# Kernel tuning notes

Hardware: AMD Instinct MI355X
Metric: run time of the kernel (lower is better)

The kernel has to match this reference:

```python
import jax, jax.numpy as jnp
import numpy as np

EPS = 1e-5

def _ln(x, g, b):
    mu = x.mean(-1, keepdims=True)
    var = ((x - mu) ** 2).mean(-1, keepdims=True)
    return (x - mu) * jax.lax.rsqrt(var + EPS) * g + b

def setup_inputs() -> dict:
    B, K, D, H, T = 64, 64, 128, 128, 4
    key = jax.random.key(0)
    ks = jax.random.split(key, 20)
    s = 0.02
    inp = {
        "slots": jax.random.normal(ks[0], (B, K, D), jnp.float32),
        "edge_probs": jax.random.uniform(ks[1], (B, K, K), jnp.float32),
        "edge_types": jax.random.uniform(ks[2], (B, K, K, T), jnp.float32),
        # f_self: LayerNorm(D) -> Linear(D,H) -> ReLU -> Linear(H,D)
        "ls_g": jnp.ones((D,), jnp.float32),
        "ls_b": jnp.zeros((D,), jnp.float32),
        "ws1": jax.random.normal(ks[3], (D, H), jnp.float32) * s,
        "bs1": jnp.zeros((H,), jnp.float32),
        "ws2": jax.random.normal(ks[4], (H, D), jnp.float32) * s,
        "bs2": jnp.zeros((D,), jnp.float32),
        # f_inter[tau]: Linear(2D,H) -> ReLU -> Linear(H,H) -> ReLU -> Linear(H,D), stacked over T
        "wi1": jax.random.normal(ks[5], (T, 2 * D, H), jnp.float32) * s,
        "bi1": jnp.zeros((T, H), jnp.float32),
        "wi2": jax.random.normal(ks[6], (T, H, H), jnp.float32) * s,
        "bi2": jnp.zeros((T, H), jnp.float32),
        "wi3": jax.random.normal(ks[7], (T, H, D), jnp.float32) * s,
        "bi3": jnp.zeros((T, D), jnp.float32),
        # update_mlp: LayerNorm(2D) -> Linear(2D,H) -> ReLU -> Linear(H,D)
        "lu_g": jnp.ones((2 * D,), jnp.float32),
        "lu_b": jnp.zeros((2 * D,), jnp.float32),
        "wu1": jax.random.normal(ks[8], (2 * D, H), jnp.float32) * s,
        "bu1": jnp.zeros((H,), jnp.float32),
        "wu2": jax.random.normal(ks[9], (H, D), jnp.float32) * s,
        "bu2": jnp.zeros((D,), jnp.float32),
    }
    return inp

NUM_MP = 2

def reference(slots, edge_probs, edge_types, ls_g, ls_b, ws1, bs1, ws2, bs2,
              wi1, bi1, wi2, bi2, wi3, bi3, lu_g, lu_b, wu1, bu1, wu2, bu2):
    B, K, D = slots.shape
    T = edge_types.shape[-1]
    h = slots
    for _ in range(NUM_MP):
        # f_self
        delta_self = jax.nn.relu(_ln(h, ls_g, ls_b) @ ws1 + bs1) @ ws2 + bs2
        # all-pairs features: cat[b,i,j] = [h[b,i] (sender), h[b,j] (receiver)]
        sender = jnp.broadcast_to(h[:, :, None, :], (B, K, K, D))
        receiver = jnp.broadcast_to(h[:, None, :, :], (B, K, K, D))
        pair = jnp.concatenate([sender, receiver], axis=-1)  # [B,K,K,2D]
        delta_inter = jnp.zeros_like(h)
        for tau in range(T):
            x = jax.nn.relu(pair @ wi1[tau] + bi1[tau])
            x = jax.nn.relu(x @ wi2[tau] + bi2[tau])
            eff = x @ wi3[tau] + bi3[tau]  # [B,K,K,D]
            w = edge_probs[..., None] * edge_types[..., tau, None]  # [B,K,K,1]
            delta_inter = delta_inter + (eff * w).sum(axis=1)  # sum over sender i
        combined = jnp.concatenate([h + delta_self, delta_inter], axis=-1)
        update = jax.nn.relu(_ln(combined, lu_g, lu_b) @ wu1 + bu1) @ wu2 + bu2
        h = h + update  # residual=True
    return h
```

## Files before the change

### kernel.cpp

```cpp
#include <hip/hip_runtime.h>
#include <hip/hip_fp16.h>

#define BATCH 64
#define KSLOT 64
#define DDIM  128
#define HDIM  128
#define TTYPE 4
#define NSLOT (BATCH*KSLOT)
#define EPSLN 1e-5f
#define YROW  544

typedef _Float16 v8h __attribute__((ext_vector_type(8)));
typedef _Float16 v4h __attribute__((ext_vector_type(4)));
typedef _Float16 v2h __attribute__((ext_vector_type(2)));
typedef float    v4f __attribute__((ext_vector_type(4)));

__device__ __forceinline__ float waveAllSum(float v) {
    #pragma unroll
    for (int m = 1; m < 64; m <<= 1) v += __shfl_xor(v, m, 64);
    return v;
}

__global__ __launch_bounds__(256) void k_wconv(
        const float* __restrict__ ws1, const float* __restrict__ wi1,
        const float* __restrict__ ws2, const float* __restrict__ wu1,
        const float* __restrict__ wu2, const float* __restrict__ wi3,
        const float* __restrict__ wi2, const float* __restrict__ bi1,
        const float* __restrict__ bi3,
        const float* __restrict__ ep, const float* __restrict__ et,
        __half* __restrict__ ws1T, __half* __restrict__ wi1catT,
        __half* __restrict__ ws2T, __half* __restrict__ wu1T,
        __half* __restrict__ wu2T, __half* __restrict__ w3catT,
        __half* __restrict__ w2T16, float* __restrict__ biascat,
        __half* __restrict__ wPre) {
    __shared__ __align__(16) float tile[128*132];
    int bx = blockIdx.x, tid = threadIdx.x;
    if (bx >= 22) {
        int bx2 = bx - 22, tau = bx2 & 3, b = bx2 >> 2;
        const float* epb = ep + (size_t)b*4096;
        const float* etb = et + (size_t)b*4096*TTYPE + tau;
        __half* dst = wPre + ((size_t)tau*BATCH + b)*4096;
        for (int idx = tid; idx < 4096; idx += 256)
            dst[idx] = __float2half(epb[idx] * etb[(size_t)idx*TTYPE]);
        return;
    }
    if (bx == 21) {
        for (int idx = tid; idx < 128*32; idx += 256) {
            int o = idx >> 5, c = idx & 31;
            w3catT[(size_t)o*YROW + 512 + c] = (c < 4) ? __float2half(bi3[c*DDIM + o]) : __float2half(0.f);
        }
        for (int idx = tid; idx < 1024; idx += 256) {
            int th = idx >> 7, o = idx & 127;
            biascat[idx] = (th & 1) ? bi1[(th>>1)*HDIM + o] : 0.f;
        }
        return;
    }
    const float* src; __half* dst; int dstride = 128, dcol = 0;
    if (bx == 0)      { src = ws1; dst = ws1T; }
    else if (bx <= 8) { int th = bx-1, tau = th>>1, half = th&1;
                        src = wi1 + ((size_t)tau*256 + half*128)*128;
                        dst = wi1catT + (size_t)th*128*128; }
    else if (bx == 9) { src = ws2; dst = ws2T; }
    else if (bx ==10) { src = wu2; dst = wu2T; }
    else if (bx <=12) { int hh = bx-11; src = wu1 + (size_t)hh*128*128;
                        dst = wu1T; dstride = 256; dcol = hh*128; }
    else if (bx <=16) { int tau = bx-13; src = wi3 + (size_t)tau*16384;
                        dst = w3catT; dstride = YROW; dcol = tau*128; }
    else              { int tau = bx-17; src = wi2 + (size_t)tau*16384;
                        dst = w2T16 + (size_t)tau*16384; }
    for (int idx = tid; idx < 4096; idx += 256) {
        int r = idx >> 5, c4 = idx & 31;
        *(float4*)&tile[r*132 + c4*4] = *(const float4*)&src[(size_t)r*128 + c4*4];
    }
    __syncthreads();
    for (int idx = tid; idx < 8192; idx += 256) {
        int n = idx >> 6, kp = idx & 63;
        __half2 p = __floats2half2_rn(tile[(2*kp)*132 + n], tile[(2*kp+1)*132 + n]);
        *(__half2*)&dst[(size_t)n*dstride + dcol + 2*kp] = p;
    }
}

#define LROW 136
__global__ __launch_bounds__(512, 4) void k_pair(
        const float* __restrict__ h,
        const __half* __restrict__ wi1catT,
        const float* __restrict__ biascat,
        const __half* __restrict__ w2T16,
        const float* __restrict__ bi2,
        const __half* __restrict__ wPre,
        __half* __restrict__ Ycat) {
    __shared__ __align__(16) _Float16 U[HDIM*LROW];
    __shared__ __align__(16) _Float16 Cs[32*LROW];
    __shared__ __align__(16) _Float16 As[KSLOT*LROW];
    __shared__ __align__(16) _Float16 wS[KSLOT*32];
    int bx = blockIdx.x;
    int jhalf = bx & 1, tau = (bx >> 1) & 3, b = bx >> 3;
    int tid = threadIdx.x, lane = tid & 63, w = tid >> 6;
    int quad = lane >> 4, n = lane & 15;
    int jt = w >> 2, oh = (w >> 1) & 1, otg = w & 1;

    v8h wreg[4];
    #pragma unroll
    for (int k2 = 0; k2 < 4; k2++) {
        int idx = tid + k2*512;
        int o = idx >> 4, seg = (idx & 15)*8;
        wreg[k2] = *(const v8h*)&w2T16[((size_t)tau*128 + o)*128 + seg];
    }
    {
        int row = tid >> 3, c0 = (tid & 7)*16;
        const float* hp = &h[(size_t)(b*KSLOT + row)*128 + c0];
        #pragma unroll
        for (int q = 0; q < 4; q++) {
            float4 f = *(const float4*)&hp[q*4];
            *(__half2*)&U[row*LROW + c0 + q*4]     = __floats2half2_rn(f.x, f.y);
            *(__half2*)&U[row*LROW + c0 + q*4 + 2] = __floats2half2_rn(f.z, f.w);
        }
    }
    if (tid < 256) {
        int i = tid >> 2, seg = (tid & 3)*8;
        *(v8h*)&wS[i*32 + seg] =
            *(const v8h*)&wPre[((size_t)tau*BATCH + b)*4096 + i*64 + jhalf*32 + seg];
    }
    __syncthreads();

    if (w < 6) {
        int isA = (w < 4);
        int rt  = isA ? w : (w - 4);
        int hrow0 = isA ? rt*16 : (jhalf*32 + rt*16);
        const __half* wb = wi1catT + (size_t)(tau*2 + (isA ? 0 : 1))*128*128;
        const float* bcp = biascat + (tau*2 + (isA ? 0 : 1))*128;
        _Float16* dst = isA ? (As + rt*16*LROW) : (Cs + rt*16*LROW);
        v8h afr[4];
        #pragma unroll
        for (int ks = 0; ks < 4; ks++)
            afr[ks] = *(const v8h*)&U[(hrow0 + n)*LROW + ks*32 + quad*8];
        #pragma unroll
        for (int ot = 0; ot < 8; ot++) {
            float b0 = bcp[ot*16 + n];
            v4f acc = (v4f){b0, b0, b0, b0};
            #pragma unroll
            for (int ks = 0; ks < 4; ks++)
                acc = __builtin_amdgcn_mfma_f32_16x16x32_f16(
                    afr[ks], *(const v8h*)&wb[(size_t)(ot*16 + n)*128 + ks*32 + quad*8], acc, 0, 0, 0);
            #pragma unroll
            for (int r = 0; r < 4; r++)
                dst[(quad*4 + r)*LROW + ot*16 + n] = (_Float16)acc[r];
        }
    }
    __syncthreads();
    #pragma unroll
    for (int k2 = 0; k2 < 4; k2++) {
        int idx = tid + k2*512;
        int o = idx >> 4, seg = (idx & 15)*8;
        *(v8h*)&U[o*LROW + seg] = wreg[k2];
    }
    __syncthreads();

    v8h bfrag[2][4];
    #pragma unroll
    for (int ot = 0; ot < 2; ot++)
        #pragma unroll
        for (int ks = 0; ks < 4; ks++)
            bfrag[ot][ks] = *(const v8h*)&U[(oh*64 + otg*32 + ot*16 + n)*LROW + ks*32 + quad*8];
    v8h cfrag[4];
    #pragma unroll
    for (int ks = 0; ks < 4; ks++)
        cfrag[ks] = *(const v8h*)&Cs[(jt*16 + n)*LROW + ks*32 + quad*8];
    v4f biasvec[2];
    #pragma unroll
    for (int ot = 0; ot < 2; ot++) {
        float b0 = bi2[tau*HDIM + oh*64 + otg*32 + ot*16 + n];
        biasvec[ot] = (v4f){b0, b0, b0, b0};
    }

    v4h yacch[2];
    #pragma unroll
    for (int ot = 0; ot < 2; ot++) yacch[ot] = (v4h){0,0,0,0};
    v4h wsacch = (v4h){0,0,0,0};
    const v8h zero8 = {0,0,0,0,0,0,0,0};
    const v4h zero4h = {0,0,0,0};

    v8h aN[4]; v4h wvN;
    #pragma unroll
    for (int ks = 0; ks < 4; ks++) aN[ks] = *(const v8h*)&As[ks*32 + quad*8];
    wvN = *(const v4h*)&wS[jt*16 + quad*4];

    for (int i = 0; i < KSLOT; ++i) {
        v8h a[4]; v4h wv = wvN;
        #pragma unroll
        for (int ks = 0; ks < 4; ks++) a[ks] = aN[ks];
        if (i < KSLOT-1) {
            #pragma unroll
            for (int ks = 0; ks < 4; ks++)
                aN[ks] = *(const v8h*)&As[(i+1)*LROW + ks*32 + quad*8];
            wvN = *(const v4h*)&wS[(i+1)*32 + jt*16 + quad*4];
        }
        v8h x1[4];
        #pragma unroll
        for (int ks = 0; ks < 4; ks++)
            x1[ks] = __builtin_elementwise_max(a[ks] + cfrag[ks], zero8);
        #pragma unroll
        for (int ot = 0; ot < 2; ot++) {
            v4f acc = __builtin_amdgcn_mfma_f32_16x16x32_f16(x1[0], bfrag[ot][0], biasvec[ot], 0, 0, 0);
            #pragma unroll
            for (int ks = 1; ks < 4; ks++)
                acc = __builtin_amdgcn_mfma_f32_16x16x32_f16(x1[ks], bfrag[ot][ks], acc, 0, 0, 0);
            v2h lo = __builtin_bit_cast(v2h, __builtin_amdgcn_cvt_pkrtz(acc[0], acc[1]));
            v2h hi = __builtin_bit_cast(v2h, __builtin_amdgcn_cvt_pkrtz(acc[2], acc[3]));
            v4h rel = {lo[0], lo[1], hi[0], hi[1]};
            rel = __builtin_elementwise_max(rel, zero4h);
            yacch[ot] = yacch[ot] + wv * rel;
        }
        wsacch = wsacch + wv;
    }

    #pragma unroll
    for (int r = 0; r < 4; r++) {
        int j = jhalf*32 + jt*16 + quad*4 + r;
        __half* yb = Ycat + (size_t)(b*KSLOT + j)*YROW + tau*128 + oh*64 + otg*32;
        #pragma unroll
        for (int ot = 0; ot < 2; ot++)
            yb[ot*16 + n] = __float2half((float)yacch[ot][r]);
    }
    if (oh == 0 && otg == 0 && n == 0) {
        #pragma unroll
        for (int r = 0; r < 4; r++) {
            int j = jhalf*32 + jt*16 + quad*4 + r;
            Ycat[(size_t)(b*KSLOT + j)*YROW + 512 + tau] = __float2half((float)wsacch[r]);
        }
    }
    if (tau == 0 && oh == 1 && otg == 1 && n == 0) {
        const v4h z4 = {0,0,0,0};
        #pragma unroll
        for (int r = 0; r < 4; r++) {
            int j = jhalf*32 + jt*16 + quad*4 + r;
            _Float16* pz = (_Float16*)(Ycat + (size_t)(b*KSLOT + j)*YROW + 516);
            #pragma unroll
            for (int c = 0; c < 28; c += 4) *(v4h*)&pz[c] = z4;
        }
    }
}

__global__ __launch_bounds__(512, 1) void k_mega(
        const __half* __restrict__ Ycat, const __half* __restrict__ w3catT,
        const float* __restrict__ ls_g, const float* __restrict__ ls_b,
        const __half* __restrict__ ws1T, const float* __restrict__ bs1,
        const __half* __restrict__ ws2T, const float* __restrict__ bs2,
        const float* __restrict__ g, const float* __restrict__ bb,
        const __half* __restrict__ wu1T, const float* __restrict__ bu1,
        const __half* __restrict__ wu2T, const float* __restrict__ bu2,
        const float* __restrict__ h, float* __restrict__ hout) {
    __shared__ __align__(16) _Float16 Ys[16*552];
    __shared__ __align__(16) float    Crow[16*260];
    __shared__ __align__(16) float    Hrow[16*132];
    __shared__ __align__(16) _Float16 Xs[16*136];
    __shared__ __align__(16) _Float16 Ts[16*136];
    __shared__ __align__(16) _Float16 Xa[16*264];
    __shared__ __align__(16) _Float16 Ut[16*136];
    int tid = threadIdx.x, lane = tid & 63, w = tid >> 6;
    int n = lane & 15, quad = lane >> 4;
    int row0 = blockIdx.x*16;
    v8h f3[17];
    #pragma unroll
    for (int ks = 0; ks < 17; ks++)
        f3[ks] = *(const v8h*)&w3catT[(size_t)(w*16 + n)*YROW + ks*32 + quad*8];
    v8h f1[8];
    #pragma unroll
    for (int ks = 0; ks < 8; ks++)
        f1[ks] = *(const v8h*)&wu1T[(size_t)(w*16 + n)*256 + ks*32 + quad*8];
    v8h f2[4], fs1[4], fs2[4];
    #pragma unroll
    for (int ks = 0; ks < 4; ks++) {
        f2[ks]  = *(const v8h*)&wu2T[(size_t)(w*16 + n)*128 + ks*32 + quad*8];
        fs1[ks] = *(const v8h*)&ws1T[(size_t)(w*16 + n)*128 + ks*32 + quad*8];
        fs2[ks] = *(const v8h*)&ws2T[(size_t)(w*16 + n)*128 + ks*32 + quad*8];
    }

    for (int u = tid; u < 1024; u += 512) {
        int r = u >> 6, seg = (u & 63)*8;
        *(v8h*)&Ys[r*552 + seg] = *(const v8h*)&Ycat[(size_t)(row0 + r)*YROW + seg];
    }
    if (tid < 64) {
        int r = tid >> 2, seg = 512 + (tid & 3)*8;
        *(v8h*)&Ys[r*552 + seg] = *(const v8h*)&Ycat[(size_t)(row0 + r)*YROW + seg];
    }
    {
        int r = tid >> 5, c4 = (tid & 31)*4;
        *(float4*)&Hrow[r*132 + c4] = *(const float4*)&h[(size_t)(row0 + r)*128 + c4];
    }
    __syncthreads();
    {
        v4f acc = (v4f){0.f,0.f,0.f,0.f};
        #pragma unroll
        for (int ks = 0; ks < 17; ks++) {
            v8h a = *(const v8h*)&Ys[n*552 + ks*32 + quad*8];
            acc = __builtin_amdgcn_mfma_f32_16x16x32_f16(a, f3[ks], acc, 0, 0, 0);
        }
        #pragma unroll
        for (int r = 0; r < 4; r++)
            Crow[(quad*4 + r)*260 + 128 + w*16 + n] = acc[r];
    }
    #pragma unroll
    for (int rr = 0; rr < 2; rr++) {
        int r = w*2 + rr;
        float x0 = Hrow[r*132 + 2*lane], x1 = Hrow[r*132 + 2*lane + 1];
        float mu = waveAllSum(x0 + x1) * (1.f/128.f);
        float d0 = x0 - mu, d1 = x1 - mu;
        float var = waveAllSum(d0*d0 + d1*d1) * (1.f/128.f);
        float rs = rsqrtf(var + EPSLN);
        float2 gv = *(const float2*)&ls_g[2*lane];
        float2 bv = *(const float2*)&ls_b[2*lane];
        *(__half2*)&Xs[r*136 + 2*lane] = __floats2half2_rn(d0*rs*gv.x + bv.x, d1*rs*gv.y + bv.y);
    }
    __syncthreads();
    {
        float b0 = bs1[w*16 + n];
        v4f acc = (v4f){b0, b0, b0, b0};
        #pragma unroll
        for (int ks = 0; ks < 4; ks++) {
            v8h a = *(const v8h*)&Xs[n*136 + ks*32 + quad*8];
            acc = __builtin_amdgcn_mfma_f32_16x16x32_f16(a, fs1[ks], acc, 0, 0, 0);
        }
        #pragma unroll
        for (int r = 0; r < 4; r++)
            Ts[(quad*4 + r)*136 + w*16 + n] = (_Float16)fmaxf(acc[r], 0.f);
    }
    __syncthreads();
    {
        float b0 = bs2[w*16 + n];
        v4f acc = (v4f){b0, b0, b0, b0};
        #pragma unroll
        for (int ks = 0; ks < 4; ks++) {
            v8h a = *(const v8h*)&Ts[n*136 + ks*32 + quad*8];
            acc = __builtin_amdgcn_mfma_f32_16x16x32_f16(a, fs2[ks], acc, 0, 0, 0);
        }
        #pragma unroll
        for (int r = 0; r < 4; r++) {
            int rr = quad*4 + r, col = w*16 + n;
            Crow[rr*260 + col] = Hrow[rr*132 + col] + acc[r];
        }
    }
    __syncthreads();
    #pragma unroll
    for (int rr = 0; rr < 2; rr++) {
        int r = w*2 + rr;
        float4 v = *(const float4*)&Crow[r*260 + 4*lane];
        float mu = waveAllSum(v.x + v.y + v.z + v.w) * (1.f/256.f);
        float d0 = v.x-mu, d1 = v.y-mu, d2 = v.z-mu, d3 = v.w-mu;
        float var = waveAllSum(d0*d0 + d1*d1 + d2*d2 + d3*d3) * (1.f/256.f);
        float rs = rsqrtf(var + EPSLN);
        float4 gv = *(const float4*)&g[4*lane];
        float4 bv = *(const float4*)&bb[4*lane];
        *(__half2*)&Xa[r*264 + 4*lane]     = __floats2half2_rn(d0*rs*gv.x + bv.x, d1*rs*gv.y + bv.y);
        *(__half2*)&Xa[r*264 + 4*lane + 2] = __floats2half2_rn(d2*rs*gv.z + bv.z, d3*rs*gv.w + bv.w);
    }
    __syncthreads();
    {
        float b0 = bu1[w*16 + n];
        v4f acc = (v4f){b0, b0, b0, b0};
        #pragma unroll
        for (int ks = 0; ks < 8; ks++) {
            v8h a = *(const v8h*)&Xa[n*264 + ks*32 + quad*8];
            acc = __builtin_amdgcn_mfma_f32_16x16x32_f16(a, f1[ks], acc, 0, 0, 0);
        }
        #pragma unroll
        for (int r = 0; r < 4; r++)
            Ut[(quad*4 + r)*136 + w*16 + n] = (_Float16)fmaxf(acc[r], 0.f);
    }
    __syncthreads();
    {
        float b0 = bu2[w*16 + n];
        v4f acc = (v4f){b0, b0, b0, b0};
        #pragma unroll
        for (int ks = 0; ks < 4; ks++) {
            v8h a = *(const v8h*)&Ut[n*136 + ks*32 + quad*8];
            acc = __builtin_amdgcn_mfma_f32_16x16x32_f16(a, f2[ks], acc, 0, 0, 0);
        }
        #pragma unroll
        for (int r = 0; r < 4; r++) {
            int rr = quad*4 + r, col = w*16 + n;
            hout[(size_t)(row0 + rr)*128 + col] = Hrow[rr*132 + col] + acc[r];
        }
    }
}

extern "C" void kernel_launch(void* const* d_in, const int* in_sizes, int n_in,
                              void* d_out, int out_size, void* d_ws, size_t ws_size,
                              hipStream_t stream) {
    const float* slots = (const float*)d_in[0];
    const float* ep    = (const float*)d_in[1];
    const float* et    = (const float*)d_in[2];
    const float* ls_g  = (const float*)d_in[3];
    const float* ls_b  = (const float*)d_in[4];
    const float* ws1   = (const float*)d_in[5];
    const float* bs1   = (const float*)d_in[6];
    const float* ws2   = (const float*)d_in[7];
    const float* bs2   = (const float*)d_in[8];
    const float* wi1   = (const float*)d_in[9];
    const float* bi1   = (const float*)d_in[10];
    const float* wi2   = (const float*)d_in[11];
    const float* bi2   = (const float*)d_in[12];
    const float* wi3   = (const float*)d_in[13];
    const float* bi3   = (const float*)d_in[14];
    const float* lu_g  = (const float*)d_in[15];
    const float* lu_b  = (const float*)d_in[16];
    const float* wu1   = (const float*)d_in[17];
    const float* bu1   = (const float*)d_in[18];
    const float* wu2   = (const float*)d_in[19];
    const float* bu2   = (const float*)d_in[20];
    float* out = (float*)d_out;

    char* p = (char*)d_ws;
    float*  h_buf   = (float*)p;   p += (size_t)NSLOT*DDIM*4;
    __half* Ycat    = (__half*)p;  p += (size_t)NSLOT*YROW*2;
    __half* wPre    = (__half*)p;  p += (size_t)TTYPE*BATCH*4096*2;
    __half* ws1T    = (__half*)p;  p += 128*128*2;
    __half* wi1catT = (__half*)p;  p += 1024*128*2;
    __half* ws2T    = (__half*)p;  p += 128*128*2;
    __half* wu1T    = (__half*)p;  p += 128*256*2;
    __half* wu2T    = (__half*)p;  p += 128*128*2;
    __half* w3catT  = (__half*)p;  p += 128*YROW*2;
    __half* w2T16   = (__half*)p;  p += 4*128*128*2;
    float*  biascat = (float*)p;   p += 1024*4;

    k_wconv<<<22 + 256, 256, 0, stream>>>(ws1, wi1, ws2, wu1, wu2, wi3, wi2, bi1, bi3,
                                          ep, et, ws1T, wi1catT, ws2T, wu1T, wu2T,
                                          w3catT, w2T16, biascat, wPre);

    for (int mp = 0; mp < 2; mp++) {
        const float* h = (mp == 0) ? slots : h_buf;
        float* hout = (mp == 0) ? h_buf : out;
        k_pair<<<BATCH*TTYPE*2, 512, 0, stream>>>(h, wi1catT, biascat, w2T16, bi2, wPre, Ycat);
        k_mega<<<NSLOT/16, 512, 0, stream>>>(Ycat, w3catT, ls_g, ls_b, ws1T, bs1, ws2T, bs2,
                                             lu_g, lu_b, wu1T, bu1, wu2T, bu2, h, hout);
    }
}
```

Baseline: 233.2 us.

## Split sender loop across waves and load W2 fragments directly from global

Reassigns the eight waves in the pair kernel so each wave covers 64 output columns (four tiles) over half of the sender range, instead of 32 columns over all 64 senders. The two sender halves are then reduced through shared memory before the output is written. The W2 fragments now go straight from global memory into registers, which removes the staging pass through the large U buffer and one barrier, and frees that shared memory. In exchange, each wave holds twice the B-fragment and accumulator registers, which may hurt occupancy under the 512x4 launch bounds, and the cross-half reduction adds two extra barriers.

```diff
diff --git a/kernel.cpp b/kernel.cpp
--- a/kernel.cpp
+++ b/kernel.cpp
@@ -89,7 +89,7 @@
         const float* __restrict__ bi2,
         const __half* __restrict__ wPre,
         __half* __restrict__ Ycat) {
-    __shared__ __align__(16) _Float16 U[HDIM*LROW];
+    __shared__ __align__(16) _Float16 hs[KSLOT*LROW];
     __shared__ __align__(16) _Float16 Cs[32*LROW];
     __shared__ __align__(16) _Float16 As[KSLOT*LROW];
     __shared__ __align__(16) _Float16 wS[KSLOT*32];
@@ -97,23 +97,23 @@
     int jhalf = bx & 1, tau = (bx >> 1) & 3, b = bx >> 3;
     int tid = threadIdx.x, lane = tid & 63, w = tid >> 6;
     int quad = lane >> 4, n = lane & 15;
-    int jt = w >> 2, oh = (w >> 1) & 1, otg = w & 1;
-
-    v8h wreg[4];
-    #pragma unroll
-    for (int k2 = 0; k2 < 4; k2++) {
-        int idx = tid + k2*512;
-        int o = idx >> 4, seg = (idx & 15)*8;
-        wreg[k2] = *(const v8h*)&w2T16[((size_t)tau*128 + o)*128 + seg];
-    }
+    int ihalf = w & 1, oh = (w >> 1) & 1, jt = w >> 2;
+
+    v8h bfrag[4][4];
+    #pragma unroll
+    for (int ot = 0; ot < 4; ot++)
+        #pragma unroll
+        for (int ks = 0; ks < 4; ks++)
+            bfrag[ot][ks] = *(const v8h*)&w2T16[((size_t)tau*128 + oh*64 + ot*16 + n)*128 + ks*32 + quad*8];
+
     {
         int row = tid >> 3, c0 = (tid & 7)*16;
         const float* hp = &h[(size_t)(b*KSLOT + row)*128 + c0];
         #pragma unroll
         for (int q = 0; q < 4; q++) {
             float4 f = *(const float4*)&hp[q*4];
-            *(__half2*)&U[row*LROW + c0 + q*4]     = __floats2half2_rn(f.x, f.y);
-            *(__half2*)&U[row*LROW + c0 + q*4 + 2] = __floats2half2_rn(f.z, f.w);
+            *(__half2*)&hs[row*LROW + c0 + q*4]     = __floats2half2_rn(f.x, f.y);
+            *(__half2*)&hs[row*LROW + c0 + q*4 + 2] = __floats2half2_rn(f.z, f.w);
         }
     }
     if (tid < 256) {
@@ -133,7 +133,7 @@
         v8h afr[4];
         #pragma unroll
         for (int ks = 0; ks < 4; ks++)
-            afr[ks] = *(const v8h*)&U[(hrow0 + n)*LROW + ks*32 + quad*8];
+            afr[ks] = *(const v8h*)&hs[(hrow0 + n)*LROW + ks*32 + quad*8];
         #pragma unroll
         for (int ot = 0; ot < 8; ot++) {
             float b0 = bcp[ot*16 + n];
@@ -148,59 +148,47 @@
         }
     }
     __syncthreads();
-    #pragma unroll
-    for (int k2 = 0; k2 < 4; k2++) {
-        int idx = tid + k2*512;
-        int o = idx >> 4, seg = (idx & 15)*8;
-        *(v8h*)&U[o*LROW + seg] = wreg[k2];
-    }
-    __syncthreads();
-
-    v8h bfrag[2][4];
-    #pragma unroll
-    for (int ot = 0; ot < 2; ot++)
-        #pragma unroll
-        for (int ks = 0; ks < 4; ks++)
-            bfrag[ot][ks] = *(const v8h*)&U[(oh*64 + otg*32 + ot*16 + n)*LROW + ks*32 + quad*8];
+
     v8h cfrag[4];
     #pragma unroll
     for (int ks = 0; ks < 4; ks++)
         cfrag[ks] = *(const v8h*)&Cs[(jt*16 + n)*LROW + ks*32 + quad*8];
-    v4f biasvec[2];
-    #pragma unroll
-    for (int ot = 0; ot < 2; ot++) {
-        float b0 = bi2[tau*HDIM + oh*64 + otg*32 + ot*16 + n];
+    v4f biasvec[4];
+    #pragma unroll
+    for (int ot = 0; ot < 4; ot++) {
+        float b0 = bi2[tau*HDIM + oh*64 + ot*16 + n];
         biasvec[ot] = (v4f){b0, b0, b0, b0};
     }
 
-    v4h yacch[2];
-    #pragma unroll
-    for (int ot = 0; ot < 2; ot++) yacch[ot] = (v4h){0,0,0,0};
+    v4h yacch[4];
+    #pragma unroll
+    for (int ot = 0; ot < 4; ot++) yacch[ot] = (v4h){0,0,0,0};
     v4h wsacch = (v4h){0,0,0,0};
     const v8h zero8 = {0,0,0,0,0,0,0,0};
     const v4h zero4h = {0,0,0,0};
 
+    int ibase = ihalf*32;
     v8h aN[4]; v4h wvN;
     #pragma unroll
-    for (int ks = 0; ks < 4; ks++) aN[ks] = *(const v8h*)&As[ks*32 + quad*8];
-    wvN = *(const v4h*)&wS[jt*16 + quad*4];
-
-    for (int i = 0; i < KSLOT; ++i) {
+    for (int ks = 0; ks < 4; ks++) aN[ks] = *(const v8h*)&As[ibase*LROW + ks*32 + quad*8];
+    wvN = *(const v4h*)&wS[ibase*32 + jt*16 + quad*4];
+
+    for (int ii = 0; ii < 32; ++ii) {
         v8h a[4]; v4h wv = wvN;
         #pragma unroll
         for (int ks = 0; ks < 4; ks++) a[ks] = aN[ks];
-        if (i < KSLOT-1) {
+        if (ii < 31) {
             #pragma unroll
             for (int ks = 0; ks < 4; ks++)
-                aN[ks] = *(const v8h*)&As[(i+1)*LROW + ks*32 + quad*8];
-            wvN = *(const v4h*)&wS[(i+1)*32 + jt*16 + quad*4];
+                aN[ks] = *(const v8h*)&As[(ibase + ii + 1)*LROW + ks*32 + quad*8];
+            wvN = *(const v4h*)&wS[(ibase + ii + 1)*32 + jt*16 + quad*4];
         }
         v8h x1[4];
         #pragma unroll
         for (int ks = 0; ks < 4; ks++)
             x1[ks] = __builtin_elementwise_max(a[ks] + cfrag[ks], zero8);
         #pragma unroll
-        for (int ot = 0; ot < 2; ot++) {
+        for (int ot = 0; ot < 4; ot++) {
             v4f acc = __builtin_amdgcn_mfma_f32_16x16x32_f16(x1[0], bfrag[ot][0], biasvec[ot], 0, 0, 0);
             #pragma unroll
             for (int ks = 1; ks < 4; ks++)
@@ -214,29 +202,44 @@
         wsacch = wsacch + wv;
     }
 
-    #pragma unroll
-    for (int r = 0; r < 4; r++) {
-        int j = jhalf*32 + jt*16 + quad*4 + r;
-        __half* yb = Ycat + (size_t)(b*KSLOT + j)*YROW + tau*128 + oh*64 + otg*32;
-        #pragma unroll
-        for (int ot = 0; ot < 2; ot++)
-            yb[ot*16 + n] = __float2half((float)yacch[ot][r]);
-    }
-    if (oh == 0 && otg == 0 && n == 0) {
+    __syncthreads();
+    v4h* sc = (v4h*)As;
+    int scbase = ((jt*2 + oh)*64 + lane)*5;
+    if (ihalf == 1) {
+        #pragma unroll
+        for (int ot = 0; ot < 4; ot++) sc[scbase + ot] = yacch[ot];
+        sc[scbase + 4] = wsacch;
+    }
+    __syncthreads();
+    if (ihalf == 0) {
+        #pragma unroll
+        for (int ot = 0; ot < 4; ot++) yacch[ot] = yacch[ot] + sc[scbase + ot];
+        wsacch = wsacch + sc[scbase + 4];
+
         #pragma unroll
         for (int r = 0; r < 4; r++) {
             int j = jhalf*32 + jt*16 + quad*4 + r;
-            Ycat[(size_t)(b*KSLOT + j)*YROW + 512 + tau] = __float2half((float)wsacch[r]);
-        }
-    }
-    if (tau == 0 && oh == 1 && otg == 1 && n == 0) {
-        const v4h z4 = {0,0,0,0};
-        #pragma unroll
-        for (int r = 0; r < 4; r++) {
-            int j = jhalf*32 + jt*16 + quad*4 + r;
-            _Float16* pz = (_Float16*)(Ycat + (size_t)(b*KSLOT + j)*YROW + 516);
-            #pragma unroll
-            for (int c = 0; c < 28; c += 4) *(v4h*)&pz[c] = z4;
+            __half* yb = Ycat + (size_t)(b*KSLOT + j)*YROW + tau*128 + oh*64;
+            #pragma unroll
+            for (int ot = 0; ot < 4; ot++)
+                yb[ot*16 + n] = __float2half((float)yacch[ot][r]);
+        }
+        if (oh == 0 && n == 0) {
+            #pragma unroll
+            for (int r = 0; r < 4; r++) {
+                int j = jhalf*32 + jt*16 + quad*4 + r;
+                Ycat[(size_t)(b*KSLOT + j)*YROW + 512 + tau] = __float2half((float)wsacch[r]);
+            }
+        }
+        if (tau == 0 && oh == 1 && n == 0) {
+            const v4h z4 = {0,0,0,0};
+            #pragma unroll
+            for (int r = 0; r < 4; r++) {
+                int j = jhalf*32 + jt*16 + quad*4 + r;
+                _Float16* pz = (_Float16*)(Ycat + (size_t)(b*KSLOT + j)*YROW + 516);
+                #pragma unroll
+                for (int c = 0; c < 28; c += 4) *(v4h*)&pz[c] = z4;
+            }
         }
     }
 }
```

Result: slower. 323.9 us (+38.9%).
